# Kernel tuning notes

Measured on AMD Instinct MI355X. Metric: run time of the kernel, lower is better.

## Reference

```python
import jax, jax.numpy as jnp
import numpy as np

B, T, C, H = 128, 256, 384, 6
HS = C // H  # 64
EPS = 1e-5


def _ln(x, g, b):
    mu = jnp.mean(x, axis=-1, keepdims=True)
    var = jnp.mean(jnp.square(x - mu), axis=-1, keepdims=True)
    return (x - mu) * jax.lax.rsqrt(var + EPS) * g + b


def setup_inputs() -> dict:
    key = jax.random.key(0)
    ks = jax.random.split(key, 12)
    s = 0.02
    return {
        "x": jax.random.normal(ks[0], (B, T, C), jnp.float32),
        "wq": jax.random.normal(ks[1], (H, C, HS), jnp.float32) * s,
        "wk": jax.random.normal(ks[2], (H, C, HS), jnp.float32) * s,
        "wv": jax.random.normal(ks[3], (H, C, HS), jnp.float32) * s,
        "w_proj": jax.random.normal(ks[4], (C, C), jnp.float32) * s,
        "b_proj": jax.random.normal(ks[5], (C,), jnp.float32) * s,
        "w1": jax.random.normal(ks[6], (C, 4 * C), jnp.float32) * s,
        "b1": jax.random.normal(ks[7], (4 * C,), jnp.float32) * s,
        "w2": jax.random.normal(ks[8], (4 * C, C), jnp.float32) * s,
        "b2": jax.random.normal(ks[9], (C,), jnp.float32) * s,
        "ln1_g": 1.0 + jax.random.normal(ks[10], (C,), jnp.float32) * s,
        "ln1_b": jnp.zeros((C,), jnp.float32),
        "ln2_g": 1.0 + jax.random.normal(ks[11], (C,), jnp.float32) * s,
        "ln2_b": jnp.zeros((C,), jnp.float32),
    }


def reference(x, wq, wk, wv, w_proj, b_proj, w1, b1, w2, b2, ln1_g, ln1_b, ln2_g, ln2_b):
    # --- attention sublayer (dropout = identity, eval mode) ---
    h = _ln(x, ln1_g, ln1_b)                              # (B,T,C)
    q = jnp.einsum("btc,hcd->bhtd", h, wq)               # (B,H,T,HS)
    k = jnp.einsum("btc,hcd->bhtd", h, wk)
    v = jnp.einsum("btc,hcd->bhtd", h, wv)
    # NOTE: original scales by n_embed**-0.5 (C), not head_size**-0.5
    wei = jnp.einsum("bhtd,bhsd->bhts", q, k) * (C ** -0.5)  # (B,H,T,T)
    tril = jnp.tril(jnp.ones((T, T), bool))
    wei = jnp.where(tril, wei, -jnp.inf)
    # NOTE: original applies softmax over torch dim=1 of (B,T,T) = query axis
    wei = jax.nn.softmax(wei, axis=2)
    attn = jnp.einsum("bhts,bhsd->bhtd", wei, v)          # (B,H,T,HS)
    attn = attn.transpose(0, 2, 1, 3).reshape(B, T, C)    # head-concat order
    x = x + attn @ w_proj + b_proj
    # --- MLP sublayer ---
    h2 = _ln(x, ln2_g, ln2_b)
    x = x + jax.nn.relu(h2 @ w1 + b1) @ w2 + b2
    return x
```

## Files before the change

kernel.cpp:

```cpp
#include <hip/hip_runtime.h>

#define BB 128
#define TT 256
#define CCH 384
#define NHH 6
#define HSZ 64
#define BTT (BB*TT)
#define QKVLD 1152

typedef unsigned short u16;
typedef unsigned int   u32;
typedef __attribute__((ext_vector_type(8))) short  short8;
typedef __attribute__((ext_vector_type(4))) float  floatx4;

__device__ __forceinline__ u16 f2bf(float f) {
  union { float f; u32 i; } v; v.f = f; u32 x = v.i;
  return (u16)((x + 0x7fffu + ((x >> 16) & 1u)) >> 16);
}
__device__ __forceinline__ float bf2f(u16 w) {
  union { u32 i; float f; } v; v.i = ((u32)w) << 16; return v.f;
}

__device__ __forceinline__ void gll16(const u16* g, u16* l) {
  __builtin_amdgcn_global_load_lds((const __attribute__((address_space(1))) void*)g,
                                   (__attribute__((address_space(3))) void*)l, 16, 0, 0);
}

template <int INBF>
__global__ __launch_bounds__(256) void ln_kernel(const void* __restrict__ xv,
                                                 const float* __restrict__ g,
                                                 const float* __restrict__ b,
                                                 u16* __restrict__ out) {
  int row = blockIdx.x * 4 + (threadIdx.x >> 6);
  int lane = threadIdx.x & 63;
  float vals[6];
  float sum = 0.f;
  if (INBF) {
    const u16* xr = (const u16*)xv + (size_t)row * CCH;
#pragma unroll
    for (int i = 0; i < 6; ++i) { vals[i] = bf2f(xr[lane + (i << 6)]); sum += vals[i]; }
  } else {
    const float* xr = (const float*)xv + (size_t)row * CCH;
#pragma unroll
    for (int i = 0; i < 6; ++i) { vals[i] = xr[lane + (i << 6)]; sum += vals[i]; }
  }
#pragma unroll
  for (int off = 32; off; off >>= 1) sum += __shfl_xor(sum, off);
  float mean = sum * (1.f / 384.f);
  float vs = 0.f;
#pragma unroll
  for (int i = 0; i < 6; ++i) { float d = vals[i] - mean; vs += d * d; }
#pragma unroll
  for (int off = 32; off; off >>= 1) vs += __shfl_xor(vs, off);
  float rinv = rsqrtf(vs * (1.f / 384.f) + 1e-5f);
  u16* orow = out + (size_t)row * CCH;
#pragma unroll
  for (int i = 0; i < 6; ++i) {
    int c = lane + (i << 6);
    orow[c] = f2bf((vals[i] - mean) * rinv * g[c] + b[c]);
  }
}

__global__ void repack_all(const float* __restrict__ wq, const float* __restrict__ wk,
                           const float* __restrict__ wv, const float* __restrict__ wproj,
                           const float* __restrict__ w1, const float* __restrict__ w2,
                           u16* __restrict__ wqkv_t, u16* __restrict__ wp_t,
                           u16* __restrict__ w1_t, u16* __restrict__ w2_t) {
  int idx = blockIdx.x * 256 + threadIdx.x;
  if (idx < 147456) {
    int n = idx / CCH, kk = idx % CCH;
    size_t src = ((size_t)(n >> 6) * CCH + kk) * 64 + (n & 63);
    wqkv_t[idx]          = f2bf(wq[src]);
    wqkv_t[idx + 147456] = f2bf(wk[src]);
    wqkv_t[idx + 294912] = f2bf(wv[src]);
  } else if (idx < 294912) {
    int i = idx - 147456;
    int n = i / CCH, kk = i % CCH;
    wp_t[i] = f2bf(wproj[(size_t)kk * CCH + n]);
  } else if (idx < 294912 + 589824) {
    int i = idx - 294912;
    int n = i / CCH, kk = i % CCH;
    w1_t[i] = f2bf(w1[(size_t)kk * 1536 + n]);
  } else if (idx < 294912 + 2 * 589824) {
    int i = idx - 294912 - 589824;
    int n = i / 1536, kk = i % 1536;
    w2_t[i] = f2bf(w2[(size_t)kk * CCH + n]);
  }
}

template <int BIAS, int RES, int RELU, int OUTBF, int RESBF>
__global__ __launch_bounds__(256, 4) void gemm_mfma(const u16* __restrict__ A,
                                                    const u16* __restrict__ W,
                                                    const float* __restrict__ bias,
                                                    const void* __restrict__ resv,
                                                    void* __restrict__ outv,
                                                    int M, int N, int K) {
  __shared__ __align__(16) u16 As[2][128 * 32];
  __shared__ __align__(16) u16 Bs[2][128 * 32];
  const int tid = threadIdx.x;
  const int lane = tid & 63;
  const int w = tid >> 6;
  const int wr = w >> 1, wc = w & 1;

  const int gx = gridDim.x;
  const int nwg = gx * gridDim.y;
  const int bid = blockIdx.y * gx + blockIdx.x;
  const int lin = (bid & 7) * (nwg >> 3) + (bid >> 3);
  const int m0 = (lin / gx) * 128, n0 = (lin % gx) * 128;

  const int lm = lane & 15, qd = lane >> 4;

  floatx4 acc[4][4];
  floatx4 zero4 = {0.f, 0.f, 0.f, 0.f};
#pragma unroll
  for (int i = 0; i < 4; ++i)
#pragma unroll
    for (int j = 0; j < 4; ++j) acc[i][j] = zero4;

  const u16* srcA[2];
  const u16* srcB[2];
#pragma unroll
  for (int c = 0; c < 2; ++c) {
    int row = 32 * w + 16 * c + (lane >> 2);
    int ch = (lane & 3) ^ ((row >> 1) & 3);
    srcA[c] = A + (size_t)(m0 + row) * K + ch * 8;
    srcB[c] = W + (size_t)(n0 + row) * K + ch * 8;
  }
  const int dAB = (32 * w) * 32;

#pragma unroll
  for (int c = 0; c < 2; ++c) gll16(srcA[c], &As[0][dAB + 512 * c]);
#pragma unroll
  for (int c = 0; c < 2; ++c) gll16(srcB[c], &Bs[0][dAB + 512 * c]);

  int ib = 0;
  for (int k0 = 0; k0 < K; k0 += 32, ib ^= 1) {
    __syncthreads();
    int kn = k0 + 32;
    if (kn < K) {
      int nb = ib ^ 1;
#pragma unroll
      for (int c = 0; c < 2; ++c) gll16(srcA[c] + kn, &As[nb][dAB + 512 * c]);
#pragma unroll
      for (int c = 0; c < 2; ++c) gll16(srcB[c] + kn, &Bs[nb][dAB + 512 * c]);
    }
    short8 af[4], bf[4];
#pragma unroll
    for (int i = 0; i < 4; ++i) {
      int rm = 64 * wr + 16 * i + lm;
      af[i] = *(const short8*)&As[ib][rm * 32 + (qd ^ ((rm >> 1) & 3)) * 8];
    }
#pragma unroll
    for (int j = 0; j < 4; ++j) {
      int rn = 64 * wc + 16 * j + lm;
      bf[j] = *(const short8*)&Bs[ib][rn * 32 + (qd ^ ((rn >> 1) & 3)) * 8];
    }
#pragma unroll
    for (int i = 0; i < 4; ++i)
#pragma unroll
      for (int j = 0; j < 4; ++j)
        acc[i][j] = __builtin_amdgcn_mfma_f32_16x16x32_bf16(af[i], bf[j], acc[i][j], 0, 0, 0);
  }

#pragma unroll
  for (int i = 0; i < 4; ++i) {
    int row0 = m0 + 64 * wr + 16 * i + qd * 4;
#pragma unroll
    for (int j = 0; j < 4; ++j) {
      int col = n0 + 64 * wc + 16 * j + lm;
      float bb = 0.f;
      if (BIAS) bb = bias[col];
#pragma unroll
      for (int r = 0; r < 4; ++r) {
        size_t idx = (size_t)(row0 + r) * N + col;
        float val = acc[i][j][r] + bb;
        if (RES) val += RESBF ? bf2f(((const u16*)resv)[idx]) : ((const float*)resv)[idx];
        if (RELU) val = fmaxf(val, 0.f);
        if (OUTBF) ((u16*)outv)[idx] = f2bf(val);
        else       ((float*)outv)[idx] = val;
      }
    }
  }
}

#define ASCALE 0.051031036307982884f

__global__ __launch_bounds__(1024) void attn_mfma(const u16* __restrict__ qkv,
                                                  u16* __restrict__ out) {
  __shared__ __align__(16) char lds_raw[36864 + 20480 + 2048];
  u16*   Ks       = (u16*)lds_raw;
  u16*   VT       = (u16*)lds_raw;
  float* partials = (float*)(lds_raw + 36864);
  u16*   stage    = (u16*)(lds_raw + 36864);
  float* gmax     = (float*)(lds_raw + 57344);
  float* linv     = (float*)(lds_raw + 58368);

  const int tid = threadIdx.x;
  const int lane = tid & 63;
  const int w = tid >> 6;
  const int lm = lane & 15, qd = lane >> 4;
  const int b = blockIdx.x / NHH, h = blockIdx.x % NHH;
  const size_t rowbase = (size_t)b * TT;
  const u16* qp = qkv + rowbase * QKVLD + h * HSZ;
  const u16* kp = qp + 384;
  const u16* vp = qp + 768;

  {
    int s = tid >> 2, c4 = tid & 3;
    const u16* src = kp + (size_t)s * QKVLD;
    *(uint4*)&Ks[s * 72 + c4 * 8]       = *(const uint4*)(src + c4 * 8);
    *(uint4*)&Ks[s * 72 + (c4 + 4) * 8] = *(const uint4*)(src + (c4 + 4) * 8);
  }
  short8 qf0, qf1;
  {
    const u16* qrow = qp + (size_t)(16 * w + lm) * QKVLD + qd * 8;
    qf0 = *(const short8*)(qrow);
    qf1 = *(const short8*)(qrow + 32);
  }
  __syncthreads();

  floatx4 acc[16];
  floatx4 zero4 = {0.f, 0.f, 0.f, 0.f};
#pragma unroll
  for (int tc = 0; tc < 16; ++tc) acc[tc] = zero4;

#pragma unroll
  for (int tc = 0; tc < 16; ++tc) {
    if (tc <= w) {
      int sr = 16 * tc + lm;
      short8 kf0 = *(const short8*)&Ks[sr * 72 + qd * 8];
      short8 kf1 = *(const short8*)&Ks[sr * 72 + 32 + qd * 8];
      acc[tc] = __builtin_amdgcn_mfma_f32_16x16x32_bf16(qf0, kf0, acc[tc], 0, 0, 0);
      acc[tc] = __builtin_amdgcn_mfma_f32_16x16x32_bf16(qf1, kf1, acc[tc], 0, 0, 0);
    }
  }

  const int rb = 16 * w + qd * 4;
  float pmax[16];
#pragma unroll
  for (int tc = 0; tc < 16; ++tc) {
    float m = -1e30f;
    if (tc <= w) {
      int sc = 16 * tc + lm;
#pragma unroll
      for (int r = 0; r < 4; ++r) {
        float vv = acc[tc][r] * ASCALE;
        vv = (rb + r >= sc) ? vv : -1e30f;
        acc[tc][r] = vv;
        m = fmaxf(m, vv);
      }
    }
    m = fmaxf(m, __shfl_xor(m, 16));
    m = fmaxf(m, __shfl_xor(m, 32));
    pmax[tc] = m;
  }
  if (lane < 16) {
#pragma unroll
    for (int tc = 0; tc < 16; ++tc) partials[w * 256 + tc * 16 + lane] = pmax[tc];
  }
  __syncthreads();
  if (tid < 256) {
    float m = partials[tid];
#pragma unroll
    for (int i = 1; i < 16; ++i) m = fmaxf(m, partials[i * 256 + tid]);
    gmax[tid] = m;
  }
  __syncthreads();

  float psum[16];
#pragma unroll
  for (int tc = 0; tc < 16; ++tc) {
    float s = 0.f;
    if (tc <= w) {
      float gm = gmax[tc * 16 + lm];
#pragma unroll
      for (int r = 0; r < 4; ++r) {
        float e = (acc[tc][r] > -1e29f) ? __expf(acc[tc][r] - gm) : 0.f;
        acc[tc][r] = e;
        s += e;
      }
    }
    s += __shfl_xor(s, 16);
    s += __shfl_xor(s, 32);
    psum[tc] = s;
  }
  if (lane < 16) {
#pragma unroll
    for (int tc = 0; tc < 16; ++tc) partials[w * 256 + tc * 16 + lane] = psum[tc];
  }
  __syncthreads();
  if (tid < 256) {
    float s = partials[tid];
#pragma unroll
    for (int i = 1; i < 16; ++i) s += partials[i * 256 + tid];
    linv[tid] = 1.f / s;
  }
  __syncthreads();

  {
    int s = tid >> 2, dg = (tid & 3) * 16;
    const u16* vrow = vp + (size_t)s * QKVLD + dg;
    u16 tmp[16];
    *(uint4*)&tmp[0] = *(const uint4*)(vrow);
    *(uint4*)&tmp[8] = *(const uint4*)(vrow + 8);
#pragma unroll
    for (int j = 0; j < 16; ++j) VT[(dg + j) * 264 + s] = tmp[j];
  }
  __syncthreads();

  u16* mst = stage + w * 640;
  floatx4 oacc[4];
#pragma unroll
  for (int nt = 0; nt < 4; ++nt) oacc[nt] = zero4;

#pragma unroll
  for (int c = 0; c < 8; ++c) {
    if (2 * c <= w) {
#pragma unroll
      for (int tt = 0; tt < 2; ++tt) {
        int tc = 2 * c + tt;
        float li = (tc <= w) ? linv[tc * 16 + lm] : 0.f;
#pragma unroll
        for (int r = 0; r < 4; ++r) {
          float pv = (tc <= w) ? acc[tc][r] * li : 0.f;
          mst[(qd * 4 + r) * 40 + tt * 16 + lm] = f2bf(pv);
        }
      }
      asm volatile("s_waitcnt lgkmcnt(0)" ::: "memory");
      short8 pf = *(const short8*)&mst[lm * 40 + qd * 8];
#pragma unroll
      for (int nt = 0; nt < 4; ++nt) {
        short8 vf = *(const short8*)&VT[(nt * 16 + lm) * 264 + c * 32 + qd * 8];
        oacc[nt] = __builtin_amdgcn_mfma_f32_16x16x32_bf16(pf, vf, oacc[nt], 0, 0, 0);
      }
      asm volatile("" ::: "memory");
    }
  }

  u16* ob = out + rowbase * CCH + h * HSZ;
#pragma unroll
  for (int nt = 0; nt < 4; ++nt) {
#pragma unroll
    for (int r = 0; r < 4; ++r) {
      int t = 16 * w + qd * 4 + r;
      ob[(size_t)t * CCH + nt * 16 + lm] = f2bf(oacc[nt][r]);
    }
  }
}

extern "C" void kernel_launch(void* const* d_in, const int* in_sizes, int n_in,
                              void* d_out, int out_size, void* d_ws, size_t ws_size,
                              hipStream_t stream) {
  const float* x     = (const float*)d_in[0];
  const float* wq    = (const float*)d_in[1];
  const float* wk    = (const float*)d_in[2];
  const float* wv    = (const float*)d_in[3];
  const float* wproj = (const float*)d_in[4];
  const float* bproj = (const float*)d_in[5];
  const float* w1    = (const float*)d_in[6];
  const float* b1    = (const float*)d_in[7];
  const float* w2    = (const float*)d_in[8];
  const float* b2    = (const float*)d_in[9];
  const float* ln1g  = (const float*)d_in[10];
  const float* ln1b  = (const float*)d_in[11];
  const float* ln2g  = (const float*)d_in[12];
  const float* ln2b  = (const float*)d_in[13];
  float* out = (float*)d_out;
  (void)in_sizes; (void)n_in; (void)out_size; (void)ws_size;

  char* ws = (char*)d_ws;
  size_t off = 0;
  auto alloc = [&](size_t bytes) -> void* {
    void* p = ws + off;
    off += (bytes + 255) & ~(size_t)255;
    return p;
  };

  u16* wqkv_t = (u16*)alloc((size_t)QKVLD * CCH * 2);
  u16* wp_t   = (u16*)alloc((size_t)CCH * CCH * 2);
  u16* w1_t   = (u16*)alloc((size_t)4 * CCH * CCH * 2);
  u16* w2_t   = (u16*)alloc((size_t)CCH * 4 * CCH * 2);
  u16*   h_b  = (u16*)alloc((size_t)BTT * CCH * 2);
  u16*   x2   = (u16*)alloc((size_t)BTT * CCH * 2);
  u16*   qkv_b = (u16*)alloc((size_t)BTT * 4 * CCH * 2);
  u16*   u_b   = qkv_b;

  repack_all<<<5760, 256, 0, stream>>>(wq, wk, wv, wproj, w1, w2,
                                       wqkv_t, wp_t, w1_t, w2_t);

  ln_kernel<0><<<BTT / 4, 256, 0, stream>>>(x, ln1g, ln1b, h_b);

  gemm_mfma<0, 0, 0, 1, 0><<<dim3(9, 256), 256, 0, stream>>>(h_b, wqkv_t, nullptr, nullptr,
                                                             qkv_b, BTT, QKVLD, CCH);
  attn_mfma<<<BB * NHH, 1024, 0, stream>>>(qkv_b, h_b);

  gemm_mfma<1, 1, 0, 1, 0><<<dim3(3, 256), 256, 0, stream>>>(h_b, wp_t, bproj, x, x2,
                                                             BTT, CCH, CCH);
  ln_kernel<1><<<BTT / 4, 256, 0, stream>>>(x2, ln2g, ln2b, h_b);

  gemm_mfma<1, 0, 1, 1, 0><<<dim3(12, 256), 256, 0, stream>>>(h_b, w1_t, b1, nullptr, u_b,
                                                              BTT, 4 * CCH, CCH);
  gemm_mfma<1, 1, 0, 0, 1><<<dim3(3, 256), 256, 0, stream>>>(u_b, w2_t, b2, x2, out,
                                                             BTT, CCH, 4 * CCH);
}
```

Before: 362.1 us.

## Rework GEMM into 256x128 tiles with triple-buffered K=64 pipeline

The MFMA GEMM moves from 128x128 tiles with 256 threads, K-step 32 and double buffering to 256x128 tiles with 512 threads, K-step 64 and a three-stage LDS ring. Global-to-LDS loads for stage t+2 are split into pieces and interleaved between four MFMA sub-blocks. Each sub-block is wrapped in s_setprio and explicit barriers, with vmcnt waits that keep one stage in flight. The goal is more operand reuse per LDS byte and better overlap of memory traffic with MFMA work. In exchange the kernel uses about 144KB of LDS, so only one workgroup fits per CU, and it adds many more barriers per K-step.

```diff
diff --git a/kernel.cpp b/kernel.cpp
--- a/kernel.cpp
+++ b/kernel.cpp
@@ -25,6 +25,9 @@
   __builtin_amdgcn_global_load_lds((const __attribute__((address_space(1))) void*)g,
                                    (__attribute__((address_space(3))) void*)l, 16, 0, 0);
 }
+
+#define BARF() do { __builtin_amdgcn_s_barrier(); asm volatile("" ::: "memory"); } while (0)
+#define LGKM0() asm volatile("s_waitcnt lgkmcnt(0)" ::: "memory")
 
 template <int INBF>
 __global__ __launch_bounds__(256) void ln_kernel(const void* __restrict__ xv,
@@ -89,14 +92,14 @@
 }
 
 template <int BIAS, int RES, int RELU, int OUTBF, int RESBF>
-__global__ __launch_bounds__(256, 4) void gemm_mfma(const u16* __restrict__ A,
+__global__ __launch_bounds__(512, 1) void gemm_mfma(const u16* __restrict__ A,
                                                     const u16* __restrict__ W,
                                                     const float* __restrict__ bias,
                                                     const void* __restrict__ resv,
                                                     void* __restrict__ outv,
                                                     int M, int N, int K) {
-  __shared__ __align__(16) u16 As[2][128 * 32];
-  __shared__ __align__(16) u16 Bs[2][128 * 32];
+  __shared__ __align__(16) u16 As[3][256 * 64];
+  __shared__ __align__(16) u16 Bs[3][128 * 64];
   const int tid = threadIdx.x;
   const int lane = tid & 63;
   const int w = tid >> 6;
@@ -106,7 +109,7 @@
   const int nwg = gx * gridDim.y;
   const int bid = blockIdx.y * gx + blockIdx.x;
   const int lin = (bid & 7) * (nwg >> 3) + (bid >> 3);
-  const int m0 = (lin / gx) * 128, n0 = (lin % gx) * 128;
+  const int m0 = (lin / gx) * 256, n0 = (lin % gx) * 128;
 
   const int lm = lane & 15, qd = lane >> 4;
 
@@ -117,49 +120,131 @@
 #pragma unroll
     for (int j = 0; j < 4; ++j) acc[i][j] = zero4;
 
-  const u16* srcA[2];
-  const u16* srcB[2];
+  const int lrow = lane >> 3, lslot = lane & 7;
+  const int schunk = lslot ^ lrow;
+  const u16* pA[4];
+  const u16* pB[2];
+#pragma unroll
+  for (int c = 0; c < 4; ++c) {
+    int row = 32 * w + 8 * c + lrow;
+    pA[c] = A + (size_t)(m0 + row) * K + schunk * 8;
+  }
 #pragma unroll
   for (int c = 0; c < 2; ++c) {
-    int row = 32 * w + 16 * c + (lane >> 2);
-    int ch = (lane & 3) ^ ((row >> 1) & 3);
-    srcA[c] = A + (size_t)(m0 + row) * K + ch * 8;
-    srcB[c] = W + (size_t)(n0 + row) * K + ch * 8;
-  }
-  const int dAB = (32 * w) * 32;
-
-#pragma unroll
-  for (int c = 0; c < 2; ++c) gll16(srcA[c], &As[0][dAB + 512 * c]);
-#pragma unroll
-  for (int c = 0; c < 2; ++c) gll16(srcB[c], &Bs[0][dAB + 512 * c]);
-
-  int ib = 0;
-  for (int k0 = 0; k0 < K; k0 += 32, ib ^= 1) {
-    __syncthreads();
-    int kn = k0 + 32;
-    if (kn < K) {
-      int nb = ib ^ 1;
-#pragma unroll
-      for (int c = 0; c < 2; ++c) gll16(srcA[c] + kn, &As[nb][dAB + 512 * c]);
-#pragma unroll
-      for (int c = 0; c < 2; ++c) gll16(srcB[c] + kn, &Bs[nb][dAB + 512 * c]);
-    }
-    short8 af[4], bf[4];
-#pragma unroll
-    for (int i = 0; i < 4; ++i) {
-      int rm = 64 * wr + 16 * i + lm;
-      af[i] = *(const short8*)&As[ib][rm * 32 + (qd ^ ((rm >> 1) & 3)) * 8];
-    }
-#pragma unroll
-    for (int j = 0; j < 4; ++j) {
-      int rn = 64 * wc + 16 * j + lm;
-      bf[j] = *(const short8*)&Bs[ib][rn * 32 + (qd ^ ((rn >> 1) & 3)) * 8];
-    }
-#pragma unroll
-    for (int i = 0; i < 4; ++i)
-#pragma unroll
-      for (int j = 0; j < 4; ++j)
-        acc[i][j] = __builtin_amdgcn_mfma_f32_16x16x32_bf16(af[i], bf[j], acc[i][j], 0, 0, 0);
+    int row = 16 * w + 8 * c + lrow;
+    pB[c] = W + (size_t)(n0 + row) * K + schunk * 8;
+  }
+
+  const int s0 = (qd ^ (lm & 7)) * 8;
+  const int s1 = ((qd ^ (lm & 7)) ^ 4) * 8;
+  const int arow = (64 * wr + lm) * 64;
+  const int brow = (64 * wc + lm) * 64;
+
+  const int nkt = K >> 6;
+
+#pragma unroll
+  for (int c = 0; c < 4; ++c) gll16(pA[c], &As[0][2048 * w + 512 * c]);
+#pragma unroll
+  for (int c = 0; c < 2; ++c) gll16(pB[c], &Bs[0][1024 * w + 512 * c]);
+#pragma unroll
+  for (int c = 0; c < 4; ++c) gll16(pA[c] + 64, &As[1][2048 * w + 512 * c]);
+#pragma unroll
+  for (int c = 0; c < 2; ++c) gll16(pB[c] + 64, &Bs[1][1024 * w + 512 * c]);
+  asm volatile("s_waitcnt vmcnt(6)" ::: "memory");
+  BARF();
+
+  int buf = 0;
+  for (int t = 0; t < nkt; ++t) {
+    const u16* Ab = As[buf];
+    const u16* Bb = Bs[buf];
+    const int sb = (buf == 0) ? 2 : buf - 1;
+    const bool stg = (t + 2 < nkt);
+    const int koff = (t + 2) << 6;
+    short8 a0, a1, b0, b1, b2, b3;
+
+    a0 = *(const short8*)&Ab[arow + 0 * 1024 + s0];
+    a1 = *(const short8*)&Ab[arow + 1 * 1024 + s0];
+    b0 = *(const short8*)&Bb[brow + 0 * 1024 + s0];
+    b1 = *(const short8*)&Bb[brow + 1 * 1024 + s0];
+    b2 = *(const short8*)&Bb[brow + 2 * 1024 + s0];
+    b3 = *(const short8*)&Bb[brow + 3 * 1024 + s0];
+    if (stg) { gll16(pA[0] + koff, &As[sb][2048 * w + 0]);
+               gll16(pA[1] + koff, &As[sb][2048 * w + 512]); }
+    BARF();
+    __builtin_amdgcn_s_setprio(1);
+    acc[0][0] = __builtin_amdgcn_mfma_f32_16x16x32_bf16(a0, b0, acc[0][0], 0, 0, 0);
+    acc[0][1] = __builtin_amdgcn_mfma_f32_16x16x32_bf16(a0, b1, acc[0][1], 0, 0, 0);
+    acc[0][2] = __builtin_amdgcn_mfma_f32_16x16x32_bf16(a0, b2, acc[0][2], 0, 0, 0);
+    acc[0][3] = __builtin_amdgcn_mfma_f32_16x16x32_bf16(a0, b3, acc[0][3], 0, 0, 0);
+    acc[1][0] = __builtin_amdgcn_mfma_f32_16x16x32_bf16(a1, b0, acc[1][0], 0, 0, 0);
+    acc[1][1] = __builtin_amdgcn_mfma_f32_16x16x32_bf16(a1, b1, acc[1][1], 0, 0, 0);
+    acc[1][2] = __builtin_amdgcn_mfma_f32_16x16x32_bf16(a1, b2, acc[1][2], 0, 0, 0);
+    acc[1][3] = __builtin_amdgcn_mfma_f32_16x16x32_bf16(a1, b3, acc[1][3], 0, 0, 0);
+    __builtin_amdgcn_s_setprio(0);
+    LGKM0();
+    BARF();
+
+    a0 = *(const short8*)&Ab[arow + 2 * 1024 + s0];
+    a1 = *(const short8*)&Ab[arow + 3 * 1024 + s0];
+    if (stg) { gll16(pA[2] + koff, &As[sb][2048 * w + 1024]);
+               gll16(pA[3] + koff, &As[sb][2048 * w + 1536]); }
+    BARF();
+    __builtin_amdgcn_s_setprio(1);
+    acc[2][0] = __builtin_amdgcn_mfma_f32_16x16x32_bf16(a0, b0, acc[2][0], 0, 0, 0);
+    acc[2][1] = __builtin_amdgcn_mfma_f32_16x16x32_bf16(a0, b1, acc[2][1], 0, 0, 0);
+    acc[2][2] = __builtin_amdgcn_mfma_f32_16x16x32_bf16(a0, b2, acc[2][2], 0, 0, 0);
+    acc[2][3] = __builtin_amdgcn_mfma_f32_16x16x32_bf16(a0, b3, acc[2][3], 0, 0, 0);
+    acc[3][0] = __builtin_amdgcn_mfma_f32_16x16x32_bf16(a1, b0, acc[3][0], 0, 0, 0);
+    acc[3][1] = __builtin_amdgcn_mfma_f32_16x16x32_bf16(a1, b1, acc[3][1], 0, 0, 0);
+    acc[3][2] = __builtin_amdgcn_mfma_f32_16x16x32_bf16(a1, b2, acc[3][2], 0, 0, 0);
+    acc[3][3] = __builtin_amdgcn_mfma_f32_16x16x32_bf16(a1, b3, acc[3][3], 0, 0, 0);
+    __builtin_amdgcn_s_setprio(0);
+    LGKM0();
+    BARF();
+
+    a0 = *(const short8*)&Ab[arow + 0 * 1024 + s1];
+    a1 = *(const short8*)&Ab[arow + 1 * 1024 + s1];
+    b0 = *(const short8*)&Bb[brow + 0 * 1024 + s1];
+    b1 = *(const short8*)&Bb[brow + 1 * 1024 + s1];
+    b2 = *(const short8*)&Bb[brow + 2 * 1024 + s1];
+    b3 = *(const short8*)&Bb[brow + 3 * 1024 + s1];
+    if (stg) gll16(pB[0] + koff, &Bs[sb][1024 * w + 0]);
+    BARF();
+    __builtin_amdgcn_s_setprio(1);
+    acc[0][0] = __builtin_amdgcn_mfma_f32_16x16x32_bf16(a0, b0, acc[0][0], 0, 0, 0);
+    acc[0][1] = __builtin_amdgcn_mfma_f32_16x16x32_bf16(a0, b1, acc[0][1], 0, 0, 0);
+    acc[0][2] = __builtin_amdgcn_mfma_f32_16x16x32_bf16(a0, b2, acc[0][2], 0, 0, 0);
+    acc[0][3] = __builtin_amdgcn_mfma_f32_16x16x32_bf16(a0, b3, acc[0][3], 0, 0, 0);
+    acc[1][0] = __builtin_amdgcn_mfma_f32_16x16x32_bf16(a1, b0, acc[1][0], 0, 0, 0);
+    acc[1][1] = __builtin_amdgcn_mfma_f32_16x16x32_bf16(a1, b1, acc[1][1], 0, 0, 0);
+    acc[1][2] = __builtin_amdgcn_mfma_f32_16x16x32_bf16(a1, b2, acc[1][2], 0, 0, 0);
+    acc[1][3] = __builtin_amdgcn_mfma_f32_16x16x32_bf16(a1, b3, acc[1][3], 0, 0, 0);
+    __builtin_amdgcn_s_setprio(0);
+    LGKM0();
+    BARF();
+
+    a0 = *(const short8*)&Ab[arow + 2 * 1024 + s1];
+    a1 = *(const short8*)&Ab[arow + 3 * 1024 + s1];
+    if (stg) gll16(pB[1] + koff, &Bs[sb][1024 * w + 512]);
+    if (t < nkt - 1) {
+      if (t <= nkt - 3) asm volatile("s_waitcnt vmcnt(6)" ::: "memory");
+      else              asm volatile("s_waitcnt vmcnt(0)" ::: "memory");
+    }
+    BARF();
+    __builtin_amdgcn_s_setprio(1);
+    acc[2][0] = __builtin_amdgcn_mfma_f32_16x16x32_bf16(a0, b0, acc[2][0], 0, 0, 0);
+    acc[2][1] = __builtin_amdgcn_mfma_f32_16x16x32_bf16(a0, b1, acc[2][1], 0, 0, 0);
+    acc[2][2] = __builtin_amdgcn_mfma_f32_16x16x32_bf16(a0, b2, acc[2][2], 0, 0, 0);
+    acc[2][3] = __builtin_amdgcn_mfma_f32_16x16x32_bf16(a0, b3, acc[2][3], 0, 0, 0);
+    acc[3][0] = __builtin_amdgcn_mfma_f32_16x16x32_bf16(a1, b0, acc[3][0], 0, 0, 0);
+    acc[3][1] = __builtin_amdgcn_mfma_f32_16x16x32_bf16(a1, b1, acc[3][1], 0, 0, 0);
+    acc[3][2] = __builtin_amdgcn_mfma_f32_16x16x32_bf16(a1, b2, acc[3][2], 0, 0, 0);
+    acc[3][3] = __builtin_amdgcn_mfma_f32_16x16x32_bf16(a1, b3, acc[3][3], 0, 0, 0);
+    __builtin_amdgcn_s_setprio(0);
+    LGKM0();
+    BARF();
+
+    buf = (buf == 2) ? 0 : buf + 1;
   }
 
 #pragma unroll
@@ -390,16 +475,16 @@
 
   ln_kernel<0><<<BTT / 4, 256, 0, stream>>>(x, ln1g, ln1b, h_b);
 
-  gemm_mfma<0, 0, 0, 1, 0><<<dim3(9, 256), 256, 0, stream>>>(h_b, wqkv_t, nullptr, nullptr,
+  gemm_mfma<0, 0, 0, 1, 0><<<dim3(9, 128), 512, 0, stream>>>(h_b, wqkv_t, nullptr, nullptr,
                                                              qkv_b, BTT, QKVLD, CCH);
   attn_mfma<<<BB * NHH, 1024, 0, stream>>>(qkv_b, h_b);
 
-  gemm_mfma<1, 1, 0, 1, 0><<<dim3(3, 256), 256, 0, stream>>>(h_b, wp_t, bproj, x, x2,
+  gemm_mfma<1, 1, 0, 1, 0><<<dim3(3, 128), 512, 0, stream>>>(h_b, wp_t, bproj, x, x2,
                                                              BTT, CCH, CCH);
   ln_kernel<1><<<BTT / 4, 256, 0, stream>>>(x2, ln2g, ln2b, h_b);
 
-  gemm_mfma<1, 0, 1, 1, 0><<<dim3(12, 256), 256, 0, stream>>>(h_b, w1_t, b1, nullptr, u_b,
+  gemm_mfma<1, 0, 1, 1, 0><<<dim3(12, 128), 512, 0, stream>>>(h_b, w1_t, b1, nullptr, u_b,
                                                               BTT, 4 * CCH, CCH);
-  gemm_mfma<1, 1, 0, 0, 1><<<dim3(3, 256), 256, 0, stream>>>(u_b, w2_t, b2, x2, out,
+  gemm_mfma<1, 1, 0, 0, 1><<<dim3(3, 128), 512, 0, stream>>>(u_b, w2_t, b2, x2, out,
                                                              BTT, CCH, 4 * CCH);
 }
```

Result: slower. 412.9 us (+14.0%).

## Fuse MLP up and down projections into one kernel with LDS-resident hidden tile

Applied to the files above, without the earlier changes.

Replaces the two MLP GEMM launches with a single kernel. Each block loads a 128-row tile of the normalized activations into swizzled LDS. It then loops over 128-column chunks of the hidden layer, computing bias+ReLU into an LDS buffer and immediately accumulating that chunk's contribution to the output projection in registers. This avoids writing and re-reading the large bf16 hidden activation through global memory and saves a launch. In exchange, every block streams the full W1 and W2 weights from global/L2 without LDS staging or software pipelining, and runs at only one 512-thread block per CU, so memory latency may be poorly hidden.

```diff
diff --git a/kernel.cpp b/kernel.cpp
--- a/kernel.cpp
+++ b/kernel.cpp
@@ -183,6 +183,108 @@
   }
 }
 
+__global__ __launch_bounds__(512, 1) void fused_mlp(const u16* __restrict__ h,
+                                                    const u16* __restrict__ w1t,
+                                                    const float* __restrict__ b1,
+                                                    const u16* __restrict__ w2t,
+                                                    const float* __restrict__ b2,
+                                                    const u16* __restrict__ x2,
+                                                    float* __restrict__ out) {
+  __shared__ __align__(16) u16 Ah[128 * 384];
+  __shared__ __align__(16) u16 Us[128 * 128];
+  const int tid = threadIdx.x;
+  const int lane = tid & 63;
+  const int w = tid >> 6;
+  const int lm = lane & 15, qd = lane >> 4;
+  const int m0 = blockIdx.x * 128;
+
+#pragma unroll
+  for (int rnd = 0; rnd < 12; ++rnd) {
+    int wbase = rnd * 4096 + w * 512;
+    int off = wbase + lane * 8;
+    int row = off / 384;
+    int slot = (off - row * 384) >> 3;
+    const u16* src = h + (size_t)(m0 + row) * 384 + ((slot ^ (row & 7)) << 3);
+    gll16(src, &Ah[wbase]);
+  }
+  asm volatile("s_waitcnt vmcnt(0)" ::: "memory");
+  __syncthreads();
+
+  floatx4 zero4 = {0.f, 0.f, 0.f, 0.f};
+  floatx4 ao[8][3];
+#pragma unroll
+  for (int i = 0; i < 8; ++i)
+#pragma unroll
+    for (int j = 0; j < 3; ++j) ao[i][j] = zero4;
+
+  const int wr1 = w >> 2, wc1 = w & 3;
+
+  for (int c = 0; c < 12; ++c) {
+    floatx4 au[4][2];
+#pragma unroll
+    for (int i = 0; i < 4; ++i) { au[i][0] = zero4; au[i][1] = zero4; }
+    const u16* w1p = w1t + (size_t)(c * 128 + 32 * wc1 + lm) * 384 + qd * 8;
+#pragma unroll
+    for (int ks = 0; ks < 12; ++ks) {
+      short8 bf0 = *(const short8*)(w1p + ks * 32);
+      short8 bf1 = *(const short8*)(w1p + 16 * 384 + ks * 32);
+      int sl = ((ks * 4 + qd) ^ (lm & 7)) << 3;
+#pragma unroll
+      for (int i = 0; i < 4; ++i) {
+        short8 af = *(const short8*)&Ah[(64 * wr1 + 16 * i + lm) * 384 + sl];
+        au[i][0] = __builtin_amdgcn_mfma_f32_16x16x32_bf16(af, bf0, au[i][0], 0, 0, 0);
+        au[i][1] = __builtin_amdgcn_mfma_f32_16x16x32_bf16(af, bf1, au[i][1], 0, 0, 0);
+      }
+    }
+    float bv0 = b1[c * 128 + 32 * wc1 + lm];
+    float bv1 = b1[c * 128 + 32 * wc1 + 16 + lm];
+#pragma unroll
+    for (int i = 0; i < 4; ++i)
+#pragma unroll
+      for (int j = 0; j < 2; ++j) {
+        int ucol = 32 * wc1 + 16 * j + lm;
+        float bv = j ? bv1 : bv0;
+#pragma unroll
+        for (int r = 0; r < 4; ++r) {
+          int urow = 64 * wr1 + 16 * i + qd * 4 + r;
+          float v = fmaxf(au[i][j][r] + bv, 0.f);
+          Us[urow * 128 + ((((ucol >> 3) ^ (urow & 7)) << 3) | (ucol & 7))] = f2bf(v);
+        }
+      }
+    __syncthreads();
+
+    const u16* w2p = w2t + (size_t)(48 * w + lm) * 1536 + c * 128 + qd * 8;
+#pragma unroll
+    for (int ks = 0; ks < 4; ++ks) {
+      short8 bb0 = *(const short8*)(w2p + ks * 32);
+      short8 bb1 = *(const short8*)(w2p + (size_t)16 * 1536 + ks * 32);
+      short8 bb2 = *(const short8*)(w2p + (size_t)32 * 1536 + ks * 32);
+      int sl = ((ks * 4 + qd) ^ (lm & 7)) << 3;
+#pragma unroll
+      for (int i = 0; i < 8; ++i) {
+        short8 uf = *(const short8*)&Us[(16 * i + lm) * 128 + sl];
+        ao[i][0] = __builtin_amdgcn_mfma_f32_16x16x32_bf16(uf, bb0, ao[i][0], 0, 0, 0);
+        ao[i][1] = __builtin_amdgcn_mfma_f32_16x16x32_bf16(uf, bb1, ao[i][1], 0, 0, 0);
+        ao[i][2] = __builtin_amdgcn_mfma_f32_16x16x32_bf16(uf, bb2, ao[i][2], 0, 0, 0);
+      }
+    }
+    __syncthreads();
+  }
+
+#pragma unroll
+  for (int i = 0; i < 8; ++i)
+#pragma unroll
+    for (int jj = 0; jj < 3; ++jj) {
+      int col = 48 * w + 16 * jj + lm;
+      float bb = b2[col];
+#pragma unroll
+      for (int r = 0; r < 4; ++r) {
+        size_t idx = (size_t)(m0 + 16 * i + qd * 4 + r) * 384 + col;
+        out[idx] = ao[i][jj][r] + bb + bf2f(x2[idx]);
+      }
+    }
+}
+
 #define ASCALE 0.051031036307982884f
 
 __global__ __launch_bounds__(1024) void attn_mfma(const u16* __restrict__ qkv,
@@ -383,7 +485,6 @@
   u16*   h_b  = (u16*)alloc((size_t)BTT * CCH * 2);
   u16*   x2   = (u16*)alloc((size_t)BTT * CCH * 2);
   u16*   qkv_b = (u16*)alloc((size_t)BTT * 4 * CCH * 2);
-  u16*   u_b   = qkv_b;
 
   repack_all<<<5760, 256, 0, stream>>>(wq, wk, wv, wproj, w1, w2,
                                        wqkv_t, wp_t, w1_t, w2_t);
@@ -398,8 +499,5 @@
                                                              BTT, CCH, CCH);
   ln_kernel<1><<<BTT / 4, 256, 0, stream>>>(x2, ln2g, ln2b, h_b);
 
-  gemm_mfma<1, 0, 1, 1, 0><<<dim3(12, 256), 256, 0, stream>>>(h_b, w1_t, b1, nullptr, u_b,
-                                                              BTT, 4 * CCH, CCH);
-  gemm_mfma<1, 1, 0, 0, 1><<<dim3(3, 256), 256, 0, stream>>>(u_b, w2_t, b2, x2, out,
-                                                             BTT, CCH, 4 * CCH);
-}
+  fused_mlp<<<256, 512, 0, stream>>>(h_b, w1_t, b1, w2_t, b2, x2, out);
+}
```

Result: slower. 388.8 us (+7.4%).

## Prepack weights into MFMA fragment order and load B directly to registers

Applied to the files above, without the earlier changes.

Weights are repacked into a per-lane MFMA fragment layout, so each wave loads its B operands straight from global memory into registers instead of staging them through LDS. The GEMM loop is manually unrolled by two with register double-buffering for B, LDS is used only for A, and launch bounds drop to 3 waves per SIMD. This removes B-tile LDS traffic and the associated LDS reads. In exchange each wave issues its own uncoalesced-reuse global loads (B tiles are reloaded by both wave rows), uses more registers, and assumes K is a multiple of 64.

```diff
diff --git a/kernel.cpp b/kernel.cpp
--- a/kernel.cpp
+++ b/kernel.cpp
@@ -67,36 +67,44 @@
                            u16* __restrict__ wqkv_t, u16* __restrict__ wp_t,
                            u16* __restrict__ w1_t, u16* __restrict__ w2_t) {
   int idx = blockIdx.x * 256 + threadIdx.x;
-  if (idx < 147456) {
-    int n = idx / CCH, kk = idx % CCH;
-    size_t src = ((size_t)(n >> 6) * CCH + kk) * 64 + (n & 63);
-    wqkv_t[idx]          = f2bf(wq[src]);
-    wqkv_t[idx + 147456] = f2bf(wk[src]);
-    wqkv_t[idx + 294912] = f2bf(wv[src]);
-  } else if (idx < 294912) {
-    int i = idx - 147456;
-    int n = i / CCH, kk = i % CCH;
-    wp_t[i] = f2bf(wproj[(size_t)kk * CCH + n]);
-  } else if (idx < 294912 + 589824) {
-    int i = idx - 294912;
-    int n = i / CCH, kk = i % CCH;
-    w1_t[i] = f2bf(w1[(size_t)kk * 1536 + n]);
-  } else if (idx < 294912 + 2 * 589824) {
-    int i = idx - 294912 - 589824;
-    int n = i / 1536, kk = i % 1536;
-    w2_t[i] = f2bf(w2[(size_t)kk * CCH + n]);
+  const int S1 = 442368;
+  const int S2 = S1 + 147456;
+  const int S3 = S2 + 589824;
+  const int S4 = S3 + 589824;
+  if (idx < S1) {
+    int i = idx, e = i & 7, l = (i >> 3) & 63, r = i >> 9;
+    int kt = r % 12, nb = r / 12;
+    int n = nb * 16 + (l & 15), k = kt * 32 + (l >> 4) * 8 + e;
+    int sel = n / 384, nn = n % 384;
+    size_t src = ((size_t)(nn >> 6) * 384 + k) * 64 + (nn & 63);
+    float v = (sel == 0) ? wq[src] : (sel == 1) ? wk[src] : wv[src];
+    wqkv_t[i] = f2bf(v);
+  } else if (idx < S2) {
+    int i = idx - S1, e = i & 7, l = (i >> 3) & 63, r = i >> 9;
+    int kt = r % 12, nb = r / 12;
+    int n = nb * 16 + (l & 15), k = kt * 32 + (l >> 4) * 8 + e;
+    wp_t[i] = f2bf(wproj[(size_t)k * 384 + n]);
+  } else if (idx < S3) {
+    int i = idx - S2, e = i & 7, l = (i >> 3) & 63, r = i >> 9;
+    int kt = r % 12, nb = r / 12;
+    int n = nb * 16 + (l & 15), k = kt * 32 + (l >> 4) * 8 + e;
+    w1_t[i] = f2bf(w1[(size_t)k * 1536 + n]);
+  } else if (idx < S4) {
+    int i = idx - S3, e = i & 7, l = (i >> 3) & 63, r = i >> 9;
+    int kt = r % 48, nb = r / 48;
+    int n = nb * 16 + (l & 15), k = kt * 32 + (l >> 4) * 8 + e;
+    w2_t[i] = f2bf(w2[(size_t)k * 384 + n]);
   }
 }
 
 template <int BIAS, int RES, int RELU, int OUTBF, int RESBF>
-__global__ __launch_bounds__(256, 4) void gemm_mfma(const u16* __restrict__ A,
-                                                    const u16* __restrict__ W,
+__global__ __launch_bounds__(256, 3) void gemm_mfma(const u16* __restrict__ A,
+                                                    const u16* __restrict__ Bp,
                                                     const float* __restrict__ bias,
                                                     const void* __restrict__ resv,
                                                     void* __restrict__ outv,
                                                     int M, int N, int K) {
   __shared__ __align__(16) u16 As[2][128 * 32];
-  __shared__ __align__(16) u16 Bs[2][128 * 32];
   const int tid = threadIdx.x;
   const int lane = tid & 63;
   const int w = tid >> 6;
@@ -109,6 +117,7 @@
   const int m0 = (lin / gx) * 128, n0 = (lin % gx) * 128;
 
   const int lm = lane & 15, qd = lane >> 4;
+  const int KT = K >> 5;
 
   floatx4 acc[4][4];
   floatx4 zero4 = {0.f, 0.f, 0.f, 0.f};
@@ -118,48 +127,68 @@
     for (int j = 0; j < 4; ++j) acc[i][j] = zero4;
 
   const u16* srcA[2];
-  const u16* srcB[2];
 #pragma unroll
   for (int c = 0; c < 2; ++c) {
     int row = 32 * w + 16 * c + (lane >> 2);
     int ch = (lane & 3) ^ ((row >> 1) & 3);
     srcA[c] = A + (size_t)(m0 + row) * K + ch * 8;
-    srcB[c] = W + (size_t)(n0 + row) * K + ch * 8;
-  }
-  const int dAB = (32 * w) * 32;
-
-#pragma unroll
-  for (int c = 0; c < 2; ++c) gll16(srcA[c], &As[0][dAB + 512 * c]);
-#pragma unroll
-  for (int c = 0; c < 2; ++c) gll16(srcB[c], &Bs[0][dAB + 512 * c]);
-
-  int ib = 0;
-  for (int k0 = 0; k0 < K; k0 += 32, ib ^= 1) {
+  }
+  const int dA = (32 * w) * 32;
+
+  const u16* bsrc[4];
+#pragma unroll
+  for (int j = 0; j < 4; ++j)
+    bsrc[j] = Bp + ((size_t)((n0 >> 4) + 4 * wc + j) * KT) * 512 + lane * 8;
+
+#pragma unroll
+  for (int c = 0; c < 2; ++c) gll16(srcA[c], &As[0][dA + 512 * c]);
+  short8 bcur[4], bnxt[4];
+#pragma unroll
+  for (int j = 0; j < 4; ++j) bcur[j] = *(const short8*)(bsrc[j]);
+
+  for (int k0 = 0; k0 < K; k0 += 64) {
     __syncthreads();
-    int kn = k0 + 32;
-    if (kn < K) {
-      int nb = ib ^ 1;
-#pragma unroll
-      for (int c = 0; c < 2; ++c) gll16(srcA[c] + kn, &As[nb][dAB + 512 * c]);
-#pragma unroll
-      for (int c = 0; c < 2; ++c) gll16(srcB[c] + kn, &Bs[nb][dAB + 512 * c]);
-    }
-    short8 af[4], bf[4];
-#pragma unroll
-    for (int i = 0; i < 4; ++i) {
-      int rm = 64 * wr + 16 * i + lm;
-      af[i] = *(const short8*)&As[ib][rm * 32 + (qd ^ ((rm >> 1) & 3)) * 8];
-    }
-#pragma unroll
-    for (int j = 0; j < 4; ++j) {
-      int rn = 64 * wc + 16 * j + lm;
-      bf[j] = *(const short8*)&Bs[ib][rn * 32 + (qd ^ ((rn >> 1) & 3)) * 8];
-    }
-#pragma unroll
-    for (int i = 0; i < 4; ++i)
-#pragma unroll
-      for (int j = 0; j < 4; ++j)
-        acc[i][j] = __builtin_amdgcn_mfma_f32_16x16x32_bf16(af[i], bf[j], acc[i][j], 0, 0, 0);
+    {
+      int kn = k0 + 32;
+      int kto = (kn >> 5) << 9;
+#pragma unroll
+      for (int j = 0; j < 4; ++j) bnxt[j] = *(const short8*)(bsrc[j] + kto);
+#pragma unroll
+      for (int c = 0; c < 2; ++c) gll16(srcA[c] + kn, &As[1][dA + 512 * c]);
+      short8 af[4];
+#pragma unroll
+      for (int i = 0; i < 4; ++i) {
+        int rm = 64 * wr + 16 * i + lm;
+        af[i] = *(const short8*)&As[0][rm * 32 + (qd ^ ((rm >> 1) & 3)) * 8];
+      }
+#pragma unroll
+      for (int i = 0; i < 4; ++i)
+#pragma unroll
+        for (int j = 0; j < 4; ++j)
+          acc[i][j] = __builtin_amdgcn_mfma_f32_16x16x32_bf16(af[i], bcur[j], acc[i][j], 0, 0, 0);
+    }
+    __syncthreads();
+    {
+      int kn = k0 + 64;
+      if (kn < K) {
+        int kto = (kn >> 5) << 9;
+#pragma unroll
+        for (int j = 0; j < 4; ++j) bcur[j] = *(const short8*)(bsrc[j] + kto);
+#pragma unroll
+        for (int c = 0; c < 2; ++c) gll16(srcA[c] + kn, &As[0][dA + 512 * c]);
+      }
+      short8 af[4];
+#pragma unroll
+      for (int i = 0; i < 4; ++i) {
+        int rm = 64 * wr + 16 * i + lm;
+        af[i] = *(const short8*)&As[1][rm * 32 + (qd ^ ((rm >> 1) & 3)) * 8];
+      }
+#pragma unroll
+      for (int i = 0; i < 4; ++i)
+#pragma unroll
+        for (int j = 0; j < 4; ++j)
+          acc[i][j] = __builtin_amdgcn_mfma_f32_16x16x32_bf16(af[i], bnxt[j], acc[i][j], 0, 0, 0);
+    }
   }
 
 #pragma unroll
@@ -385,7 +414,7 @@
   u16*   qkv_b = (u16*)alloc((size_t)BTT * 4 * CCH * 2);
   u16*   u_b   = qkv_b;
 
-  repack_all<<<5760, 256, 0, stream>>>(wq, wk, wv, wproj, w1, w2,
+  repack_all<<<6912, 256, 0, stream>>>(wq, wk, wv, wproj, w1, w2,
                                        wqkv_t, wp_t, w1_t, w2_t);
 
   ln_kernel<0><<<BTT / 4, 256, 0, stream>>>(x, ln1g, ln1b, h_b);
```

After: 339.6 us. 1.07x faster.
